# Performance work log

Measured on AMD Instinct MI355X. Metric: run time of the kernel, lower is better.

The kernel has to match this reference:

```python
import jax, jax.numpy as jnp
import numpy as np

N, D, H, E, TOP_K = 8192, 1024, 2048, 8, 2


def setup_inputs() -> dict:
    key = jax.random.key(0)
    ks = jax.random.split(key, 5)
    s_in = 1.0 / np.sqrt(D)
    s_hid = 1.0 / np.sqrt(H)
    return {
        "x": jax.random.normal(ks[0], (N, D), dtype=jnp.float32),
        "Wg": jax.random.normal(ks[1], (D, E), dtype=jnp.float32) * s_in,
        "bg": jnp.zeros((E,), dtype=jnp.float32),
        "W1": jax.random.normal(ks[2], (E, D, H), dtype=jnp.float32) * s_in,
        "b1": jnp.zeros((E, H), dtype=jnp.float32),
        "W2": jax.random.normal(ks[3], (E, H, H), dtype=jnp.float32) * s_hid,
        "b2": jnp.zeros((E, H), dtype=jnp.float32),
    }


def _moe_forward(x, Wg, bg, W1, b1, W2, b2):
    # Router
    gate_logits = x @ Wg + bg                      # [N, E]
    gate_probs = jax.nn.softmax(gate_logits, axis=-1)
    topk_probs, topk_idx = jax.lax.top_k(gate_probs, TOP_K)  # [N, K]
    topk_probs = topk_probs / (jnp.sum(topk_probs, axis=-1, keepdims=True) + 1e-8)
    rows = jnp.arange(x.shape[0])[:, None]
    gate_mask = jnp.zeros_like(gate_probs).at[rows, topk_idx].set(topk_probs)  # [N, E]

    # Dense all-expert compute (dropout is identity in eval)
    h = jax.nn.relu(jnp.einsum('nd,edh->neh', x, W1) + b1)    # [N, E, H]
    expert_out = jnp.einsum('neh,ehk->nek', h, W2) + b2        # [N, E, H]

    output = jnp.einsum('neh,ne->nh', expert_out, gate_mask)   # [N, H]
    return output, gate_probs, gate_mask


def reference(x, Wg, bg, W1, b1, W2, b2):
    return _moe_forward(x, Wg, bg, W1, b1, W2, b2)
```

## Files before the change

kernel.cpp:

```cpp
#include <hip/hip_runtime.h>

#define N_TOK 8192
#define DIM   1024
#define HID   2048
#define NEXP  8
#define TOPK  2
#define BM 128
#define BN 128
#define BK 64
#define NTHREADS 256
#define MAXROWS (N_TOK*TOPK + NEXP*BM)
#define MAXRT   (MAXROWS/BM)
#define NT_COL  (HID/BN)
#define NPAIR   (N_TOK*TOPK)

#define CVT1_NB (32*16*8)
#define CVT2_NB (32*32*8)
#define ROUT_NB (N_TOK/4)
#define PREP_NB (CVT1_NB + CVT2_NB + ROUT_NB)

typedef float f32x4 __attribute__((ext_vector_type(4)));
typedef short bf16x8 __attribute__((ext_vector_type(8)));

static __device__ __forceinline__ unsigned short f2bf(float f){
    union { float f; unsigned u; } v; v.f = f;
    unsigned r = v.u + 0x7FFFu + ((v.u >> 16) & 1u);
    return (unsigned short)(r >> 16);
}
static __device__ __forceinline__ float bf2f(unsigned short u){
    union { unsigned u; float f; } v; v.u = ((unsigned)u) << 16;
    return v.f;
}

static __device__ __forceinline__ void gload_lds16(const void* g, void* l){
    __builtin_amdgcn_global_load_lds((const __attribute__((address_space(1))) void*)g,
                                     (__attribute__((address_space(3))) void*)l,
                                     16, 0, 0);
}

__global__ __launch_bounds__(256) void prep_moe(
    const float* __restrict__ W1, unsigned short* __restrict__ W1t,
    const float* __restrict__ W2, unsigned short* __restrict__ W2t,
    const float* __restrict__ x,  const float* __restrict__ Wg,
    const float* __restrict__ bg,
    float* __restrict__ gate_probs, float* __restrict__ gate_mask,
    int* __restrict__ tk_e, float* __restrict__ tk_w)
{
    __shared__ float tile[64][65];
    const int bid = blockIdx.x;

    if (bid < CVT1_NB + CVT2_NB) {
        const float* src; unsigned short* dst; int R, C, c0, r0;
        if (bid < CVT1_NB) {
            int p = bid;
            c0 = (p & 31) * 64; r0 = ((p >> 5) & 15) * 64; int z = p >> 9;
            src = W1 + (size_t)z*DIM*HID; dst = W1t + (size_t)z*DIM*HID;
            R = DIM; C = HID;
        } else {
            int p = bid - CVT1_NB;
            c0 = (p & 31) * 64; r0 = ((p >> 5) & 31) * 64; int z = p >> 10;
            src = W2 + (size_t)z*HID*HID; dst = W2t + (size_t)z*HID*HID;
            R = HID; C = HID;
        }
        const int tq = threadIdx.x & 15, tr = threadIdx.x >> 4;
        #pragma unroll
        for (int p = 0; p < 4; ++p) {
            int row = p*16 + tr;
            float4 v = *(const float4*)(src + (size_t)(r0 + row) * C + c0 + tq*4);
            tile[row][tq*4+0] = v.x; tile[row][tq*4+1] = v.y;
            tile[row][tq*4+2] = v.z; tile[row][tq*4+3] = v.w;
        }
        __syncthreads();
        #pragma unroll
        for (int p = 0; p < 4; ++p) {
            int orow = p*16 + tr;
            ushort4 o;
            o.x = f2bf(tile[tq*4+0][orow]);
            o.y = f2bf(tile[tq*4+1][orow]);
            o.z = f2bf(tile[tq*4+2][orow]);
            o.w = f2bf(tile[tq*4+3][orow]);
            *(ushort4*)(dst + (size_t)(c0 + orow) * R + r0 + tq*4) = o;
        }
        return;
    }

    const int lane = threadIdx.x & 63;
    const int n = (bid - CVT1_NB - CVT2_NB) * 4 + (threadIdx.x >> 6);
    const float* xr = x + (size_t)n * DIM;

    float acc[NEXP];
    #pragma unroll
    for (int e = 0; e < NEXP; ++e) acc[e] = 0.f;
    #pragma unroll
    for (int i = 0; i < DIM/256; ++i) {
        int d4 = i*256 + lane*4;
        float4 xv = *(const float4*)(xr + d4);
        const float xs[4] = {xv.x, xv.y, xv.z, xv.w};
        #pragma unroll
        for (int j = 0; j < 4; ++j) {
            const float4* wrow = (const float4*)(Wg + (size_t)(d4 + j) * NEXP);
            float4 w0 = wrow[0], w1 = wrow[1];
            acc[0] += xs[j]*w0.x; acc[1] += xs[j]*w0.y;
            acc[2] += xs[j]*w0.z; acc[3] += xs[j]*w0.w;
            acc[4] += xs[j]*w1.x; acc[5] += xs[j]*w1.y;
            acc[6] += xs[j]*w1.z; acc[7] += xs[j]*w1.w;
        }
    }
    #pragma unroll
    for (int off = 32; off > 0; off >>= 1) {
        #pragma unroll
        for (int e = 0; e < NEXP; ++e) acc[e] += __shfl_xor(acc[e], off, 64);
    }
    float lgt[NEXP];
    float mx = acc[0] + bg[0];
    #pragma unroll
    for (int e = 0; e < NEXP; ++e) { lgt[e] = acc[e] + bg[e]; mx = fmaxf(mx, lgt[e]); }
    float s = 0.f;
    #pragma unroll
    for (int e = 0; e < NEXP; ++e) { lgt[e] = expf(lgt[e] - mx); s += lgt[e]; }
    float inv = 1.f / s;
    #pragma unroll
    for (int e = 0; e < NEXP; ++e) lgt[e] *= inv;

    int i1 = 0;
    #pragma unroll
    for (int e = 1; e < NEXP; ++e) if (lgt[e] > lgt[i1]) i1 = e;
    int i2 = (i1 == 0) ? 1 : 0;
    #pragma unroll
    for (int e = 0; e < NEXP; ++e) if (e != i1 && lgt[e] > lgt[i2]) i2 = e;
    float wsum = lgt[i1] + lgt[i2] + 1e-8f;
    float w1n = lgt[i1] / wsum, w2n = lgt[i2] / wsum;

    if (lane < NEXP) {
        gate_probs[(size_t)n*NEXP + lane] = lgt[lane];
        gate_mask [(size_t)n*NEXP + lane] = (lane == i1) ? w1n : (lane == i2) ? w2n : 0.f;
    }
    if (lane == 0) {
        tk_e[n*TOPK]   = i1; tk_e[n*TOPK+1] = i2;
        tk_w[n*TOPK]   = w1n; tk_w[n*TOPK+1] = w2n;
    }
}

__global__ __launch_bounds__(1024) void assign_moe(
    const int* __restrict__ tk_e,
    int* __restrict__ slot_row, int* __restrict__ pair_token,
    int* __restrict__ sched_e, int* __restrict__ sched_row,
    int* __restrict__ total_tiles)
{
    __shared__ int whist[16][NEXP];
    __shared__ int wbase[16][NEXP];
    const int w = threadIdx.x >> 6, lane = threadIdx.x & 63;
    const int PW = NPAIR / 16;
    const unsigned long long below = ((unsigned long long)1 << lane) - 1;

    for (int i = threadIdx.x; i < MAXROWS; i += 1024) pair_token[i] = -1;

    int h[NEXP] = {0,0,0,0,0,0,0,0};
    for (int i = 0; i < PW/64; ++i) {
        int e = tk_e[w*PW + i*64 + lane];
        #pragma unroll
        for (int ee = 0; ee < NEXP; ++ee)
            h[ee] += __popcll(__ballot(e == ee));
    }
    if (lane == 0) {
        #pragma unroll
        for (int ee = 0; ee < NEXP; ++ee) whist[w][ee] = h[ee];
    }
    __syncthreads();

    if (threadIdx.x == 0) {
        int base = 0, t = 0, ebase[NEXP];
        for (int e = 0; e < NEXP; ++e) {
            int c = 0;
            for (int ww = 0; ww < 16; ++ww) c += whist[ww][e];
            ebase[e] = base;
            int nt = (c + BM - 1) / BM;
            for (int i = 0; i < nt; ++i) { sched_e[t] = e; sched_row[t] = base + i*BM; ++t; }
            base += nt * BM;
        }
        *total_tiles = t;
        for (int e = 0; e < NEXP; ++e) {
            int r = ebase[e];
            for (int ww = 0; ww < 16; ++ww) { wbase[ww][e] = r; r += whist[ww][e]; }
        }
    }
    __syncthreads();

    int run[NEXP];
    #pragma unroll
    for (int ee = 0; ee < NEXP; ++ee) run[ee] = wbase[w][ee];
    for (int i = 0; i < PW/64; ++i) {
        int idx = w*PW + i*64 + lane;
        int e = tk_e[idx];
        int myslot = 0;
        #pragma unroll
        for (int ee = 0; ee < NEXP; ++ee) {
            unsigned long long m = __ballot(e == ee);
            if (e == ee) myslot = run[ee] + __popcll(m & below);
            run[ee] += __popcll(m);
        }
        slot_row[idx] = myslot;
        pair_token[myslot] = idx;
    }
}

__global__ __launch_bounds__(256) void gather_moe(
    const float* __restrict__ x, const int* __restrict__ slot_row,
    unsigned short* __restrict__ Xg)
{
    const int n = blockIdx.x;
    const int r0 = slot_row[n*TOPK], r1 = slot_row[n*TOPK+1];
    float4 xv = ((const float4*)(x + (size_t)n * DIM))[threadIdx.x];
    ushort4 b;
    b.x = f2bf(xv.x); b.y = f2bf(xv.y); b.z = f2bf(xv.z); b.w = f2bf(xv.w);
    ((ushort4*)(Xg + (size_t)r0 * DIM))[threadIdx.x] = b;
    ((ushort4*)(Xg + (size_t)r1 * DIM))[threadIdx.x] = b;
}

#define G_MFMA(MH, NH, BF) do {                                              \
    __builtin_amdgcn_s_setprio(1);                                           \
    _Pragma("unroll")                                                        \
    for (int mi = 0; mi < 2; ++mi)                                           \
        _Pragma("unroll")                                                    \
        for (int nb = 0; nb < 2; ++nb)                                       \
            _Pragma("unroll")                                                \
            for (int kk = 0; kk < 2; ++kk)                                   \
                acc[(MH)*2+mi][(NH)*2+nb] =                                  \
                    __builtin_amdgcn_mfma_f32_16x16x32_bf16(                 \
                        af[mi][kk], BF[nb][kk], acc[(MH)*2+mi][(NH)*2+nb],   \
                        0, 0, 0);                                            \
    __builtin_amdgcn_s_setprio(0);                                           \
} while (0)

template<int K, int MODE>
__global__ __launch_bounds__(256, 3) void gemm_moe(
    const unsigned short* __restrict__ A,
    const unsigned short* __restrict__ Bt,
    const float* __restrict__ bias,
    const int* __restrict__ sched_e, const int* __restrict__ sched_row,
    const int* __restrict__ total_tiles,
    unsigned short* __restrict__ Out,
    const int* __restrict__ pair_token)
{
    const int nwg  = gridDim.x * gridDim.y;
    const int orig = blockIdx.y * gridDim.x + blockIdx.x;
    const int q = nwg >> 3, r8 = nwg & 7, xcd = orig & 7, lin = orig >> 3;
    const int wg = (xcd < r8 ? xcd*(q+1) : r8*(q+1) + (xcd-r8)*q) + lin;
    const int rt = wg / NT_COL, ct = wg % NT_COL;
    if (rt >= *total_tiles) return;

    const int e    = sched_e[rt];
    const int row0 = sched_row[rt];
    const int col0 = ct * BN;
    const unsigned short* Be = Bt + (size_t)e * HID * K;

    __shared__ __align__(1024) char lds[32768];
    char* ldsA = lds;
    char* ldsB = lds + 16384;

    const int tid  = threadIdx.x;
    const int wv   = tid >> 6, lane = tid & 63;
    const int wr   = wv >> 1,  wc   = wv & 1;
    const int lrow = lane & 15, lg  = lane >> 4;
    const int sr   = lane >> 3, si  = lane & 7;
    const int gc16 = si ^ sr;

    const unsigned short* Ab = A  + (size_t)row0 * K + gc16 * 8;
    const unsigned short* Bb = Be + (size_t)col0 * K + gc16 * 8;

    f32x4 acc[4][4] = {};
    bf16x8 af[2][2], b0f[2][2], b1f[2][2];

    auto STAGE_A = [&](int h, int t) {
        char* dst = ldsA + h*8192;
        #pragma unroll
        for (int j = 0; j < 2; ++j) {
            int c = wv*2 + j;
            int idx = c*8 + sr;
            int r = ((idx>>5)<<6) + h*32 + (idx&31);
            gload_lds16(Ab + (size_t)r * K + t*BK, dst + c*1024);
        }
    };
    auto STAGE_B = [&](int h, int t) {
        char* dst = ldsB + h*8192;
        #pragma unroll
        for (int j = 0; j < 2; ++j) {
            int c = wv*2 + j;
            int idx = c*8 + sr;
            int gcol = ((idx>>5)<<6) + h*32 + (idx&31);
            gload_lds16(Bb + (size_t)gcol * K + t*BK, dst + c*1024);
        }
    };
    auto RD_A = [&](int mh) {
        const char* base = ldsA + mh*8192;
        #pragma unroll
        for (int mi = 0; mi < 2; ++mi) {
            int idx = wr*32 + mi*16 + lrow;
            #pragma unroll
            for (int kk = 0; kk < 2; ++kk) {
                int s = (kk*4 + lg) ^ (idx & 7);
                af[mi][kk] = *(const bf16x8*)(base + idx*128 + s*16);
            }
        }
    };
    auto RD_B = [&](int nh, bf16x8 (*bf)[2]) {
        const char* base = ldsB + nh*8192;
        #pragma unroll
        for (int nb = 0; nb < 2; ++nb) {
            int idx = wc*32 + nb*16 + lrow;
            #pragma unroll
            for (int kk = 0; kk < 2; ++kk) {
                int s = (kk*4 + lg) ^ (idx & 7);
                bf[nb][kk] = *(const bf16x8*)(base + idx*128 + s*16);
            }
        }
    };
    auto BARRIER = [&]() {
        __builtin_amdgcn_sched_barrier(0);
        __builtin_amdgcn_s_barrier();
        __builtin_amdgcn_sched_barrier(0);
    };
    auto LGKM0 = [&]() {
        asm volatile("s_waitcnt lgkmcnt(0)" ::: "memory");
        __builtin_amdgcn_sched_barrier(0);
    };

    constexpr int NT = K / BK;
    static_assert(NT >= 2, "need >=2 K-tiles");

    STAGE_A(0, 0); STAGE_B(0, 0); STAGE_B(1, 0); STAGE_A(1, 0);
    asm volatile("s_waitcnt vmcnt(4)" ::: "memory");
    BARRIER();

    for (int t = 0; t < NT; ++t) {
        const bool pf = (t + 1 < NT);
        RD_A(0); RD_B(0, b0f);
        BARRIER(); LGKM0();
        G_MFMA(0,0,b0f);
        asm volatile("s_waitcnt vmcnt(2)" ::: "memory");
        BARRIER();
        RD_B(1, b1f);
        if (pf) { STAGE_A(0, t+1); STAGE_B(0, t+1); }
        BARRIER(); LGKM0();
        G_MFMA(0,1,b1f);
        if (pf) { asm volatile("s_waitcnt vmcnt(4)" ::: "memory"); }
        else    { asm volatile("s_waitcnt vmcnt(0)" ::: "memory"); }
        BARRIER();
        RD_A(1);
        if (pf) STAGE_B(1, t+1);
        BARRIER(); LGKM0();
        G_MFMA(1,0,b0f);
        BARRIER();
        if (pf) STAGE_A(1, t+1);
        BARRIER();
        G_MFMA(1,1,b1f);
        if (pf) { asm volatile("s_waitcnt vmcnt(4)" ::: "memory"); BARRIER(); }
    }

    if constexpr (MODE == 0) {
        #pragma unroll
        for (int n = 0; n < 4; ++n) {
            int col = col0 + wc*64 + ((n>>1)<<5) + ((n&1)<<4) + lrow;
            float bv = bias[(size_t)e*HID + col];
            #pragma unroll
            for (int m = 0; m < 4; ++m) {
                int rb = row0 + wr*64 + ((m>>1)<<5) + ((m&1)<<4) + lg*4;
                #pragma unroll
                for (int j = 0; j < 4; ++j) {
                    float v = fmaxf(acc[m][n][j] + bv, 0.f);
                    Out[(size_t)(rb + j) * HID + col] = f2bf(v);
                }
            }
        }
    } else {
        float bv[4]; int cols[4];
        #pragma unroll
        for (int n = 0; n < 4; ++n) {
            cols[n] = col0 + wc*64 + ((n>>1)<<5) + ((n&1)<<4) + lrow;
            bv[n] = bias[(size_t)e*HID + cols[n]];
        }
        #pragma unroll
        for (int m = 0; m < 4; ++m) {
            #pragma unroll
            for (int j = 0; j < 4; ++j) {
                int r = row0 + wr*64 + ((m>>1)<<5) + ((m&1)<<4) + lg*4 + j;
                int pair = pair_token[r];
                if (pair < 0) continue;
                size_t prow = (size_t)(pair & 1) * N_TOK + (pair >> 1);
                #pragma unroll
                for (int n = 0; n < 4; ++n)
                    Out[prow * HID + cols[n]] = f2bf(acc[m][n][j] + bv[n]);
            }
        }
    }
}

__global__ __launch_bounds__(256) void combine_moe(
    const unsigned short* __restrict__ P, const float* __restrict__ tk_w,
    float* __restrict__ out)
{
    for (int n = blockIdx.x; n < N_TOK; n += gridDim.x) {
        const float w0 = tk_w[n*2], w1 = tk_w[n*2+1];
        const int c = threadIdx.x * 8;
        bf16x8 a = *(const bf16x8*)(P + (size_t)n * HID + c);
        bf16x8 b = *(const bf16x8*)(P + (size_t)(N_TOK + n) * HID + c);
        float4 o0, o1;
        float* op = &o0.x;
        #pragma unroll
        for (int i = 0; i < 4; ++i)
            op[i] = w0 * bf2f((unsigned short)a[i]) + w1 * bf2f((unsigned short)b[i]);
        float* op1 = &o1.x;
        #pragma unroll
        for (int i = 0; i < 4; ++i)
            op1[i] = w0 * bf2f((unsigned short)a[4+i]) + w1 * bf2f((unsigned short)b[4+i]);
        float4* dst = (float4*)(out + (size_t)n * HID + c);
        dst[0] = o0; dst[1] = o1;
    }
}

extern "C" void kernel_launch(void* const* d_in, const int* in_sizes, int n_in,
                              void* d_out, int out_size, void* d_ws, size_t ws_size,
                              hipStream_t stream)
{
    const float* x  = (const float*)d_in[0];
    const float* Wg = (const float*)d_in[1];
    const float* bg = (const float*)d_in[2];
    const float* W1 = (const float*)d_in[3];
    const float* b1 = (const float*)d_in[4];
    const float* W2 = (const float*)d_in[5];
    const float* b2 = (const float*)d_in[6];

    float* out        = (float*)d_out;
    float* gate_probs = out + (size_t)N_TOK * HID;
    float* gate_mask  = gate_probs + (size_t)N_TOK * NEXP;

    char* p = (char*)d_ws;
    auto carve = [&](size_t bytes) { char* r = p; p += (bytes + 255) & ~(size_t)255; return r; };
    unsigned short* W2t = (unsigned short*)carve((size_t)NEXP*HID*HID*2);
    unsigned short* Hb  = (unsigned short*)carve((size_t)MAXROWS*HID*2);
    unsigned short* W1t = (unsigned short*)carve((size_t)NEXP*DIM*HID*2);
    unsigned short* Xg  = (unsigned short*)carve((size_t)MAXROWS*DIM*2);
    unsigned short* P   = W1t;
    int*   pair_token = (int*)  carve((size_t)MAXROWS*4);
    int*   slot_row   = (int*)  carve((size_t)NPAIR*4);
    int*   tk_e       = (int*)  carve((size_t)NPAIR*4);
    float* tk_w       = (float*)carve((size_t)NPAIR*4);
    int*   sched_e    = (int*)  carve(1024);
    int*   sched_row  = (int*)  carve(1024);
    int*   total_tiles= (int*)  carve(256);

    prep_moe<<<PREP_NB, 256, 0, stream>>>(W1, W1t, W2, W2t, x, Wg, bg,
                                          gate_probs, gate_mask, tk_e, tk_w);
    assign_moe<<<1, 1024, 0, stream>>>(tk_e, slot_row, pair_token,
                                       sched_e, sched_row, total_tiles);
    gather_moe<<<N_TOK, 256, 0, stream>>>(x, slot_row, Xg);
    gemm_moe<DIM, 0><<<dim3(MAXRT, NT_COL), NTHREADS, 0, stream>>>(
        Xg, W1t, b1, sched_e, sched_row, total_tiles, Hb, nullptr);
    gemm_moe<HID, 1><<<dim3(MAXRT, NT_COL), NTHREADS, 0, stream>>>(
        Hb, W2t, b2, sched_e, sched_row, total_tiles, P, pair_token);
    combine_moe<<<2048, 256, 0, stream>>>(P, tk_w, out);
}
```

Measured before the change: 351.0 us.

## Move W2 bf16 transpose-convert into the first expert GEMM launch

The W2 fp32-to-bf16 transpose conversion moves out of the prep kernel and becomes extra trailing blocks of the first grouped GEMM launch, which reuse that kernel's shared memory as the tile buffer. The aim is to overlap this bandwidth-bound conversion with the compute-bound first GEMM and shorten the serial prep stage. The GEMM grid becomes 1D and the XCD remap now uses a fixed block count. The risk is that the conversion blocks compete with GEMM tiles for CUs and bandwidth, and early-exiting GEMM blocks may leave the conversion blocks to run last as a tail.

```diff
diff --git a/kernel.cpp b/kernel.cpp
--- a/kernel.cpp
+++ b/kernel.cpp
@@ -13,11 +13,12 @@
 #define MAXRT   (MAXROWS/BM)
 #define NT_COL  (HID/BN)
 #define NPAIR   (N_TOK*TOPK)
+#define GEMM_NB (MAXRT*NT_COL)
 
 #define CVT1_NB (32*16*8)
+#define ROUT_NB (N_TOK/4)
+#define PREP_NB (CVT1_NB + ROUT_NB)
 #define CVT2_NB (32*32*8)
-#define ROUT_NB (N_TOK/4)
-#define PREP_NB (CVT1_NB + CVT2_NB + ROUT_NB)
 
 typedef float f32x4 __attribute__((ext_vector_type(4)));
 typedef short bf16x8 __attribute__((ext_vector_type(8)));
@@ -38,9 +39,33 @@
                                      16, 0, 0);
 }
 
+static __device__ __forceinline__ void cvt_tile64(
+    float (*tile)[65], const float* __restrict__ src,
+    unsigned short* __restrict__ dst, int R, int C, int r0, int c0, int tid)
+{
+    const int tq = tid & 15, tr = tid >> 4;
+    #pragma unroll
+    for (int p = 0; p < 4; ++p) {
+        int row = p*16 + tr;
+        float4 v = *(const float4*)(src + (size_t)(r0 + row) * C + c0 + tq*4);
+        tile[row][tq*4+0] = v.x; tile[row][tq*4+1] = v.y;
+        tile[row][tq*4+2] = v.z; tile[row][tq*4+3] = v.w;
+    }
+    __syncthreads();
+    #pragma unroll
+    for (int p = 0; p < 4; ++p) {
+        int orow = p*16 + tr;
+        ushort4 o;
+        o.x = f2bf(tile[tq*4+0][orow]);
+        o.y = f2bf(tile[tq*4+1][orow]);
+        o.z = f2bf(tile[tq*4+2][orow]);
+        o.w = f2bf(tile[tq*4+3][orow]);
+        *(ushort4*)(dst + (size_t)(c0 + orow) * R + r0 + tq*4) = o;
+    }
+}
+
 __global__ __launch_bounds__(256) void prep_moe(
     const float* __restrict__ W1, unsigned short* __restrict__ W1t,
-    const float* __restrict__ W2, unsigned short* __restrict__ W2t,
     const float* __restrict__ x,  const float* __restrict__ Wg,
     const float* __restrict__ bg,
     float* __restrict__ gate_probs, float* __restrict__ gate_mask,
@@ -49,43 +74,16 @@
     __shared__ float tile[64][65];
     const int bid = blockIdx.x;
 
-    if (bid < CVT1_NB + CVT2_NB) {
-        const float* src; unsigned short* dst; int R, C, c0, r0;
-        if (bid < CVT1_NB) {
-            int p = bid;
-            c0 = (p & 31) * 64; r0 = ((p >> 5) & 15) * 64; int z = p >> 9;
-            src = W1 + (size_t)z*DIM*HID; dst = W1t + (size_t)z*DIM*HID;
-            R = DIM; C = HID;
-        } else {
-            int p = bid - CVT1_NB;
-            c0 = (p & 31) * 64; r0 = ((p >> 5) & 31) * 64; int z = p >> 10;
-            src = W2 + (size_t)z*HID*HID; dst = W2t + (size_t)z*HID*HID;
-            R = HID; C = HID;
-        }
-        const int tq = threadIdx.x & 15, tr = threadIdx.x >> 4;
-        #pragma unroll
-        for (int p = 0; p < 4; ++p) {
-            int row = p*16 + tr;
-            float4 v = *(const float4*)(src + (size_t)(r0 + row) * C + c0 + tq*4);
-            tile[row][tq*4+0] = v.x; tile[row][tq*4+1] = v.y;
-            tile[row][tq*4+2] = v.z; tile[row][tq*4+3] = v.w;
-        }
-        __syncthreads();
-        #pragma unroll
-        for (int p = 0; p < 4; ++p) {
-            int orow = p*16 + tr;
-            ushort4 o;
-            o.x = f2bf(tile[tq*4+0][orow]);
-            o.y = f2bf(tile[tq*4+1][orow]);
-            o.z = f2bf(tile[tq*4+2][orow]);
-            o.w = f2bf(tile[tq*4+3][orow]);
-            *(ushort4*)(dst + (size_t)(c0 + orow) * R + r0 + tq*4) = o;
-        }
+    if (bid < CVT1_NB) {
+        int p = bid;
+        int c0 = (p & 31) * 64, r0 = ((p >> 5) & 15) * 64, z = p >> 9;
+        cvt_tile64(tile, W1 + (size_t)z*DIM*HID, W1t + (size_t)z*DIM*HID,
+                   DIM, HID, r0, c0, threadIdx.x);
         return;
     }
 
     const int lane = threadIdx.x & 63;
-    const int n = (bid - CVT1_NB - CVT2_NB) * 4 + (threadIdx.x >> 6);
+    const int n = (bid - CVT1_NB) * 4 + (threadIdx.x >> 6);
     const float* xr = x + (size_t)n * DIM;
 
     float acc[NEXP];
@@ -240,10 +238,26 @@
     const int* __restrict__ sched_e, const int* __restrict__ sched_row,
     const int* __restrict__ total_tiles,
     unsigned short* __restrict__ Out,
-    const int* __restrict__ pair_token)
-{
-    const int nwg  = gridDim.x * gridDim.y;
-    const int orig = blockIdx.y * gridDim.x + blockIdx.x;
+    const int* __restrict__ pair_token,
+    const float* __restrict__ cvt_src,
+    unsigned short* __restrict__ cvt_dst)
+{
+    __shared__ __align__(1024) char lds[32768];
+    const int bid = blockIdx.x;
+
+    if constexpr (MODE == 0) {
+        if (bid >= GEMM_NB) {
+            int p = bid - GEMM_NB;
+            int c0 = (p & 31)*64, r0 = ((p >> 5) & 31)*64, z = p >> 10;
+            cvt_tile64((float(*)[65])lds,
+                       cvt_src + (size_t)z*HID*HID, cvt_dst + (size_t)z*HID*HID,
+                       HID, HID, r0, c0, threadIdx.x);
+            return;
+        }
+    }
+
+    const int nwg  = GEMM_NB;
+    const int orig = bid;
     const int q = nwg >> 3, r8 = nwg & 7, xcd = orig & 7, lin = orig >> 3;
     const int wg = (xcd < r8 ? xcd*(q+1) : r8*(q+1) + (xcd-r8)*q) + lin;
     const int rt = wg / NT_COL, ct = wg % NT_COL;
@@ -254,7 +268,6 @@
     const int col0 = ct * BN;
     const unsigned short* Be = Bt + (size_t)e * HID * K;
 
-    __shared__ __align__(1024) char lds[32768];
     char* ldsA = lds;
     char* ldsB = lds + 16384;
 
@@ -449,14 +462,14 @@
     int*   sched_row  = (int*)  carve(1024);
     int*   total_tiles= (int*)  carve(256);
 
-    prep_moe<<<PREP_NB, 256, 0, stream>>>(W1, W1t, W2, W2t, x, Wg, bg,
+    prep_moe<<<PREP_NB, 256, 0, stream>>>(W1, W1t, x, Wg, bg,
                                           gate_probs, gate_mask, tk_e, tk_w);
     assign_moe<<<1, 1024, 0, stream>>>(tk_e, slot_row, pair_token,
                                        sched_e, sched_row, total_tiles);
     gather_moe<<<N_TOK, 256, 0, stream>>>(x, slot_row, Xg);
-    gemm_moe<DIM, 0><<<dim3(MAXRT, NT_COL), NTHREADS, 0, stream>>>(
-        Xg, W1t, b1, sched_e, sched_row, total_tiles, Hb, nullptr);
-    gemm_moe<HID, 1><<<dim3(MAXRT, NT_COL), NTHREADS, 0, stream>>>(
-        Hb, W2t, b2, sched_e, sched_row, total_tiles, P, pair_token);
+    gemm_moe<DIM, 0><<<GEMM_NB + CVT2_NB, NTHREADS, 0, stream>>>(
+        Xg, W1t, b1, sched_e, sched_row, total_tiles, Hb, nullptr, W2, W2t);
+    gemm_moe<HID, 1><<<GEMM_NB, NTHREADS, 0, stream>>>(
+        Hb, W2t, b2, sched_e, sched_row, total_tiles, P, pair_token, nullptr, nullptr);
     combine_moe<<<2048, 256, 0, stream>>>(P, tk_w, out);
 }
```

After: 368.6 us. 5.0% more time.
